# Performance work log

Measured on AMD Instinct MI355X. Metric: run time of the kernel, lower is better.

Reference implementation:

```python
import jax, jax.numpy as jnp
import numpy as np

EMBED_DIM = 1024
HEAD_NUM = 16
HEAD_DIM = 64


def setup_inputs() -> dict:
    key = jax.random.key(0)
    ks = jax.random.split(key, 9)
    B, S = 4, 4096
    sc = 1.0 / np.sqrt(HEAD_DIM)
    scf = 1.0 / np.sqrt(HEAD_NUM * HEAD_DIM)
    return {
        "value": jax.random.normal(ks[0], (B, S, EMBED_DIM), jnp.float32),
        "key": jax.random.normal(ks[1], (B, S, EMBED_DIM), jnp.float32),
        "query": jax.random.normal(ks[2], (B, S, EMBED_DIM), jnp.float32),
        "Wv": jax.random.normal(ks[3], (HEAD_DIM, HEAD_DIM), jnp.float32) * sc,
        "bv": jnp.zeros((HEAD_DIM,), jnp.float32),
        "Wk": jax.random.normal(ks[4], (HEAD_DIM, HEAD_DIM), jnp.float32) * sc,
        "bk": jnp.zeros((HEAD_DIM,), jnp.float32),
        "Wq": jax.random.normal(ks[5], (HEAD_DIM, HEAD_DIM), jnp.float32) * sc,
        "bq": jnp.zeros((HEAD_DIM,), jnp.float32),
        "Wfc": jax.random.normal(ks[6], (EMBED_DIM, HEAD_NUM * HEAD_DIM), jnp.float32) * scf,
        "bfc": jnp.zeros((EMBED_DIM,), jnp.float32),
    }


def reference(value, key, query, Wv, bv, Wk, bk, Wq, bq, Wfc, bfc):
    B, S, _ = value.shape
    H, D = HEAD_NUM, HEAD_DIM
    # reshape to [B, S, H, D]; per-head linear shares weights across heads
    v = value.reshape(B, S, H, D) @ Wv.T + bv
    k = key.reshape(B, S, H, D) @ Wk.T + bk
    q = query.reshape(B, S, H, D) @ Wq.T + bq
    # NOTE: faithful to original: attention over HEAD axis per position -> [B,S,H,H]
    energy = jnp.einsum("bshd,bsgd->bshg", q, k)
    attn = jax.nn.softmax(energy / jnp.sqrt(jnp.asarray(D, energy.dtype)), axis=-1)
    out = jnp.einsum("bshg,bsgd->bshd", attn, v).reshape(B, S, H * D)
    return out @ Wfc.T + bfc
```

## Files before the change

kernel.cpp:

```cpp
#include <hip/hip_runtime.h>
#include <hip/hip_bf16.h>

#define AS1 __attribute__((address_space(1)))
#define AS3 __attribute__((address_space(3)))

typedef __attribute__((ext_vector_type(8))) short bf16x8v;
typedef __attribute__((ext_vector_type(4))) short bf16x4v;
typedef __attribute__((ext_vector_type(4))) float f32x4;

__device__ __forceinline__ short f2bf(float f) {
  __hip_bfloat16 h = __float2bfloat16(f);
  return *reinterpret_cast<short*>(&h);
}
__device__ __forceinline__ bf16x4v cvt4(f32x4 v) {
  bf16x4v r; r[0]=f2bf(v[0]); r[1]=f2bf(v[1]); r[2]=f2bf(v[2]); r[3]=f2bf(v[3]);
  return r;
}
__device__ __forceinline__ bf16x8v cvt8(float4 a, float4 b) {
  bf16x8v r;
  r[0]=f2bf(a.x); r[1]=f2bf(a.y); r[2]=f2bf(a.z); r[3]=f2bf(a.w);
  r[4]=f2bf(b.x); r[5]=f2bf(b.y); r[6]=f2bf(b.z); r[7]=f2bf(b.w);
  return r;
}

__global__ void prep_kernel(const float* __restrict__ Wq, const float* __restrict__ Wk,
                            const float* __restrict__ Wv, const float* __restrict__ Wfc,
                            __hip_bfloat16* __restrict__ Wqb, __hip_bfloat16* __restrict__ Wkb,
                            __hip_bfloat16* __restrict__ Wvb, __hip_bfloat16* __restrict__ Wfcb)
{
  int i = blockIdx.x * blockDim.x + threadIdx.x;
  if (i < 64 * 64) {
    Wqb[i] = __float2bfloat16(Wq[i]);
    Wkb[i] = __float2bfloat16(Wk[i]);
    Wvb[i] = __float2bfloat16(Wv[i]);
  }
  for (int j = i; j < 1024 * 1024; j += gridDim.x * blockDim.x)
    Wfcb[j] = __float2bfloat16(Wfc[j]);
}

__global__ __launch_bounds__(256, 2) void attn_kernel(
    const float* __restrict__ Vin, const float* __restrict__ Kin,
    const float* __restrict__ Qin,
    const __hip_bfloat16* __restrict__ Wvb, const __hip_bfloat16* __restrict__ Wkb,
    const __hip_bfloat16* __restrict__ Wqb,
    const float* __restrict__ bv, const float* __restrict__ bk,
    const float* __restrict__ bq,
    __hip_bfloat16* __restrict__ Xout)
{
  const int wid = threadIdx.x >> 6, lane = threadIdx.x & 63;
  const int lo = lane & 15, hi = lane >> 4;
  const int tok0 = (blockIdx.x * 4 + wid) * 4;

  bf16x8v wqf[4][2], wkf[4][2], wvf[4][2];
#pragma unroll
  for (int i = 0; i < 4; ++i)
#pragma unroll
    for (int ks = 0; ks < 2; ++ks) {
      const int off = (i * 16 + lo) * 64 + ks * 32 + hi * 8;
      wqf[i][ks] = *(const bf16x8v*)(Wqb + off);
      wkf[i][ks] = *(const bf16x8v*)(Wkb + off);
      wvf[i][ks] = *(const bf16x8v*)(Wvb + off);
    }
  float4 bq4[4], bk4[4]; float bvv[4];
#pragma unroll
  for (int i = 0; i < 4; ++i) {
    bq4[i] = *(const float4*)(bq + i * 16 + hi * 4);
    bk4[i] = *(const float4*)(bk + i * 16 + hi * 4);
    bvv[i] = bv[i * 16 + lo];
  }

#pragma unroll 1
  for (int tl = 0; tl < 4; ++tl) {
    const size_t tb = (size_t)(tok0 + tl) * 1024;
    const float* qp = Qin + tb + lo * 64 + hi * 8;
    const float* kp = Kin + tb + lo * 64 + hi * 8;
    const float* vp = Vin + tb + lo * 64 + hi * 8;
    float4 qa0 = *(const float4*)(qp),      qb0 = *(const float4*)(qp + 4);
    float4 qa1 = *(const float4*)(qp + 32), qb1 = *(const float4*)(qp + 36);
    float4 ka0 = *(const float4*)(kp),      kb0 = *(const float4*)(kp + 4);
    float4 ka1 = *(const float4*)(kp + 32), kb1 = *(const float4*)(kp + 36);
    float4 va0 = *(const float4*)(vp),      vb0 = *(const float4*)(vp + 4);
    float4 va1 = *(const float4*)(vp + 32), vb1 = *(const float4*)(vp + 36);
    bf16x8v xq[2] = { cvt8(qa0, qb0), cvt8(qa1, qb1) };
    bf16x8v xk[2] = { cvt8(ka0, kb0), cvt8(ka1, kb1) };
    bf16x8v xv[2] = { cvt8(va0, vb0), cvt8(va1, vb1) };

    f32x4 qt[4], kt[4], vc[4];
#pragma unroll
    for (int i = 0; i < 4; ++i) {
      f32x4 aq = { bq4[i].x, bq4[i].y, bq4[i].z, bq4[i].w };
      aq = __builtin_amdgcn_mfma_f32_16x16x32_bf16(wqf[i][0], xq[0], aq, 0, 0, 0);
      aq = __builtin_amdgcn_mfma_f32_16x16x32_bf16(wqf[i][1], xq[1], aq, 0, 0, 0);
      qt[i] = aq;
      f32x4 ak = { bk4[i].x, bk4[i].y, bk4[i].z, bk4[i].w };
      ak = __builtin_amdgcn_mfma_f32_16x16x32_bf16(wkf[i][0], xk[0], ak, 0, 0, 0);
      ak = __builtin_amdgcn_mfma_f32_16x16x32_bf16(wkf[i][1], xk[1], ak, 0, 0, 0);
      kt[i] = ak;
    }
#pragma unroll
    for (int i = 0; i < 4; ++i) {
      f32x4 av = { bvv[i], bvv[i], bvv[i], bvv[i] };
      av = __builtin_amdgcn_mfma_f32_16x16x32_bf16(xv[0], wvf[i][0], av, 0, 0, 0);
      av = __builtin_amdgcn_mfma_f32_16x16x32_bf16(xv[1], wvf[i][1], av, 0, 0, 0);
      vc[i] = av;
    }

    f32x4 e = { 0.f, 0.f, 0.f, 0.f };
#pragma unroll
    for (int di = 0; di < 4; ++di)
      e = __builtin_amdgcn_mfma_f32_16x16x16bf16_1k(cvt4(kt[di]), cvt4(qt[di]), e, 0, 0, 0);

    float mx = fmaxf(fmaxf(e[0], e[1]), fmaxf(e[2], e[3]));
    mx = fmaxf(mx, __shfl_xor(mx, 16));
    mx = fmaxf(mx, __shfl_xor(mx, 32));
    float p0 = __expf((e[0] - mx) * 0.125f);
    float p1 = __expf((e[1] - mx) * 0.125f);
    float p2 = __expf((e[2] - mx) * 0.125f);
    float p3 = __expf((e[3] - mx) * 0.125f);
    float s = p0 + p1 + p2 + p3;
    s += __shfl_xor(s, 16);
    s += __shfl_xor(s, 32);
    const float inv = 1.0f / s;
    bf16x4v pa;
    pa[0] = f2bf(p0 * inv); pa[1] = f2bf(p1 * inv);
    pa[2] = f2bf(p2 * inv); pa[3] = f2bf(p3 * inv);

    __hip_bfloat16* xo = Xout + tb + (size_t)hi * 4 * 64 + lo;
#pragma unroll
    for (int ni = 0; ni < 4; ++ni) {
      f32x4 z = { 0.f, 0.f, 0.f, 0.f };
      z = __builtin_amdgcn_mfma_f32_16x16x16bf16_1k(pa, cvt4(vc[ni]), z, 0, 0, 0);
#pragma unroll
      for (int j = 0; j < 4; ++j)
        xo[j * 64 + ni * 16] = __float2bfloat16(z[j]);
    }
  }
}

__global__ __launch_bounds__(256) void gemm_kernel(
    const __hip_bfloat16* __restrict__ A,
    const __hip_bfloat16* __restrict__ B,
    const float* __restrict__ bias, float* __restrict__ C)
{
  constexpr int K = 1024, N = 1024;
  __shared__ __hip_bfloat16 Asm[128 * 64];
  __shared__ __hip_bfloat16 Bsm[128 * 64];
  const int tid = threadIdx.x, wid = tid >> 6, lane = tid & 63;
  const int bm = blockIdx.x >> 3, bn = blockIdx.x & 7;
  const int m0 = bm * 128, n0 = bn * 128;
  const int wr = wid >> 1, wc = wid & 1;

  f32x4 acc[4][4];
#pragma unroll
  for (int i = 0; i < 4; ++i)
#pragma unroll
    for (int j = 0; j < 4; ++j) acc[i][j] = (f32x4){0.f, 0.f, 0.f, 0.f};

  const int lrow = lane >> 3;
  const int gcol = ((lane & 7) ^ lrow) * 8;

  for (int kt = 0; kt < K / 64; ++kt) {
    const int k0 = kt * 64;
    __syncthreads();
#pragma unroll
    for (int c = 0; c < 4; ++c) {
      const int ca = wid * 4 + c;
      const int row = ca * 8 + lrow;
      __builtin_amdgcn_global_load_lds(
          (const AS1 void*)(A + (size_t)(m0 + row) * K + k0 + gcol),
          (AS3 void*)((char*)Asm + ca * 1024), 16, 0, 0);
      __builtin_amdgcn_global_load_lds(
          (const AS1 void*)(B + (size_t)(n0 + row) * K + k0 + gcol),
          (AS3 void*)((char*)Bsm + ca * 1024), 16, 0, 0);
    }
    asm volatile("s_waitcnt vmcnt(0)" ::: "memory");
    __syncthreads();

#pragma unroll
    for (int ks = 0; ks < 2; ++ks) {
      bf16x8v af[4], bfr[4];
#pragma unroll
      for (int mi = 0; mi < 4; ++mi) {
        const int arow = wr * 64 + mi * 16 + (lane & 15);
        const int slot = (ks * 4 + (lane >> 4)) ^ (arow & 7);
        af[mi] = *(const bf16x8v*)((const char*)Asm + arow * 128 + slot * 16);
      }
#pragma unroll
      for (int ni = 0; ni < 4; ++ni) {
        const int brow = wc * 64 + ni * 16 + (lane & 15);
        const int slot = (ks * 4 + (lane >> 4)) ^ (brow & 7);
        bfr[ni] = *(const bf16x8v*)((const char*)Bsm + brow * 128 + slot * 16);
      }
#pragma unroll
      for (int mi = 0; mi < 4; ++mi)
#pragma unroll
        for (int ni = 0; ni < 4; ++ni)
          acc[mi][ni] = __builtin_amdgcn_mfma_f32_16x16x32_bf16(
              af[mi], bfr[ni], acc[mi][ni], 0, 0, 0);
    }
  }

#pragma unroll
  for (int mi = 0; mi < 4; ++mi) {
    const int r0 = m0 + wr * 64 + mi * 16 + (lane >> 4) * 4;
#pragma unroll
    for (int ni = 0; ni < 4; ++ni) {
      const int c = n0 + wc * 64 + ni * 16 + (lane & 15);
      const float bs = bias[c];
#pragma unroll
      for (int j = 0; j < 4; ++j)
        C[(size_t)(r0 + j) * N + c] = acc[mi][ni][j] + bs;
    }
  }
}

extern "C" void kernel_launch(void* const* d_in, const int* in_sizes, int n_in,
                              void* d_out, int out_size, void* d_ws, size_t ws_size,
                              hipStream_t stream)
{
  const float* value = (const float*)d_in[0];
  const float* key   = (const float*)d_in[1];
  const float* query = (const float*)d_in[2];
  const float* Wv  = (const float*)d_in[3];
  const float* bv  = (const float*)d_in[4];
  const float* Wk  = (const float*)d_in[5];
  const float* bk  = (const float*)d_in[6];
  const float* Wq  = (const float*)d_in[7];
  const float* bq  = (const float*)d_in[8];
  const float* Wfc = (const float*)d_in[9];
  const float* bfc = (const float*)d_in[10];
  float* out = (float*)d_out;

  char* ws = (char*)d_ws;
  __hip_bfloat16* Xb   = (__hip_bfloat16*)ws;
  __hip_bfloat16* Wfcb = (__hip_bfloat16*)(ws + 33554432);
  __hip_bfloat16* Wqb  = (__hip_bfloat16*)(ws + 33554432 + 2097152);
  __hip_bfloat16* Wkb  = Wqb + 4096;
  __hip_bfloat16* Wvb  = Wkb + 4096;

  prep_kernel<<<4096, 256, 0, stream>>>(Wq, Wk, Wv, Wfc, Wqb, Wkb, Wvb, Wfcb);
  attn_kernel<<<1024, 256, 0, stream>>>(value, key, query, Wvb, Wkb, Wqb,
                                        bv, bk, bq, Xb);
  gemm_kernel<<<1024, 256, 0, stream>>>(Xb, Wfcb, bfc, out);
}
```

Measured before the change: 118.9 us.

## Stage per-head weights in LDS as pre-swizzled fragments to cut register pressure

The prep kernel now writes the Q/K/V weight matrices in an MFMA-fragment order. The attention kernel copies them into shared memory with global_load_lds and reads fragments from LDS each iteration, instead of holding 48 bf16x8 registers per lane. This frees VGPRs so more waves can run; the launch bound minimum of 2 blocks is dropped. It also splits the energy accumulation into two independent MFMA chains, moves the V projection after the softmax, and reorders the GEMM block index so consecutive blocks share the same N tile. The cost is extra LDS traffic per token and a barrier at kernel start.

```diff
diff --git a/kernel.cpp b/kernel.cpp
--- a/kernel.cpp
+++ b/kernel.cpp
@@ -7,6 +7,9 @@
 typedef __attribute__((ext_vector_type(8))) short bf16x8v;
 typedef __attribute__((ext_vector_type(4))) short bf16x4v;
 typedef __attribute__((ext_vector_type(4))) float f32x4;
+
+#define MFMA32 __builtin_amdgcn_mfma_f32_16x16x32_bf16
+#define MFMA16 __builtin_amdgcn_mfma_f32_16x16x16bf16_1k
 
 __device__ __forceinline__ short f2bf(float f) {
   __hip_bfloat16 h = __float2bfloat16(f);
@@ -25,42 +28,42 @@
 
 __global__ void prep_kernel(const float* __restrict__ Wq, const float* __restrict__ Wk,
                             const float* __restrict__ Wv, const float* __restrict__ Wfc,
-                            __hip_bfloat16* __restrict__ Wqb, __hip_bfloat16* __restrict__ Wkb,
-                            __hip_bfloat16* __restrict__ Wvb, __hip_bfloat16* __restrict__ Wfcb)
+                            __hip_bfloat16* __restrict__ Wfrag,
+                            __hip_bfloat16* __restrict__ Wfcb)
 {
   int i = blockIdx.x * blockDim.x + threadIdx.x;
   if (i < 64 * 64) {
-    Wqb[i] = __float2bfloat16(Wq[i]);
-    Wkb[i] = __float2bfloat16(Wk[i]);
-    Wvb[i] = __float2bfloat16(Wv[i]);
+    const int r = i >> 6, c = i & 63;
+    const int dst = (((r >> 4) * 2 + (c >> 5)) * 512) +
+                    ((((c >> 3) & 3) * 16 + (r & 15)) * 8) + (c & 7);
+    Wfrag[dst]        = __float2bfloat16(Wq[i]);
+    Wfrag[4096 + dst] = __float2bfloat16(Wk[i]);
+    Wfrag[8192 + dst] = __float2bfloat16(Wv[i]);
   }
   for (int j = i; j < 1024 * 1024; j += gridDim.x * blockDim.x)
     Wfcb[j] = __float2bfloat16(Wfc[j]);
 }
 
-__global__ __launch_bounds__(256, 2) void attn_kernel(
+__global__ __launch_bounds__(256) void attn_kernel(
     const float* __restrict__ Vin, const float* __restrict__ Kin,
     const float* __restrict__ Qin,
-    const __hip_bfloat16* __restrict__ Wvb, const __hip_bfloat16* __restrict__ Wkb,
-    const __hip_bfloat16* __restrict__ Wqb,
+    const __hip_bfloat16* __restrict__ Wfrag,
     const float* __restrict__ bv, const float* __restrict__ bk,
     const float* __restrict__ bq,
     __hip_bfloat16* __restrict__ Xout)
 {
+  __shared__ __hip_bfloat16 wlds[12288];
   const int wid = threadIdx.x >> 6, lane = threadIdx.x & 63;
   const int lo = lane & 15, hi = lane >> 4;
   const int tok0 = (blockIdx.x * 4 + wid) * 4;
-
-  bf16x8v wqf[4][2], wkf[4][2], wvf[4][2];
-#pragma unroll
-  for (int i = 0; i < 4; ++i)
-#pragma unroll
-    for (int ks = 0; ks < 2; ++ks) {
-      const int off = (i * 16 + lo) * 64 + ks * 32 + hi * 8;
-      wqf[i][ks] = *(const bf16x8v*)(Wqb + off);
-      wkf[i][ks] = *(const bf16x8v*)(Wkb + off);
-      wvf[i][ks] = *(const bf16x8v*)(Wvb + off);
-    }
+  const int xoff = lo * 64 + hi * 8;
+
+#pragma unroll
+  for (int c = 0; c < 6; ++c) {
+    const int ch = wid * 6 + c;
+    __builtin_amdgcn_global_load_lds((const AS1 void*)(Wfrag + ch * 512 + lane * 8),
+                                     (AS3 void*)(wlds + ch * 512), 16, 0, 0);
+  }
   float4 bq4[4], bk4[4]; float bvv[4];
 #pragma unroll
   for (int i = 0; i < 4; ++i) {
@@ -68,47 +71,53 @@
     bk4[i] = *(const float4*)(bk + i * 16 + hi * 4);
     bvv[i] = bv[i * 16 + lo];
   }
+  asm volatile("s_waitcnt vmcnt(0)" ::: "memory");
+  __syncthreads();
+
+  const char* wq_b = (const char*)wlds;
+  const char* wk_b = (const char*)(wlds + 4096);
+  const char* wv_b = (const char*)(wlds + 8192);
+  const int lb = lane * 16;
 
 #pragma unroll 1
-  for (int tl = 0; tl < 4; ++tl) {
-    const size_t tb = (size_t)(tok0 + tl) * 1024;
-    const float* qp = Qin + tb + lo * 64 + hi * 8;
-    const float* kp = Kin + tb + lo * 64 + hi * 8;
-    const float* vp = Vin + tb + lo * 64 + hi * 8;
+  for (int n = 0; n < 4; ++n) {
+    const size_t tb = (size_t)(tok0 + n) * 1024;
+    const float* qp = Qin + tb + xoff;
+    const float* kp = Kin + tb + xoff;
+    const float* vp = Vin + tb + xoff;
     float4 qa0 = *(const float4*)(qp),      qb0 = *(const float4*)(qp + 4);
     float4 qa1 = *(const float4*)(qp + 32), qb1 = *(const float4*)(qp + 36);
     float4 ka0 = *(const float4*)(kp),      kb0 = *(const float4*)(kp + 4);
     float4 ka1 = *(const float4*)(kp + 32), kb1 = *(const float4*)(kp + 36);
     float4 va0 = *(const float4*)(vp),      vb0 = *(const float4*)(vp + 4);
     float4 va1 = *(const float4*)(vp + 32), vb1 = *(const float4*)(vp + 36);
-    bf16x8v xq[2] = { cvt8(qa0, qb0), cvt8(qa1, qb1) };
-    bf16x8v xk[2] = { cvt8(ka0, kb0), cvt8(ka1, kb1) };
-    bf16x8v xv[2] = { cvt8(va0, vb0), cvt8(va1, vb1) };
-
-    f32x4 qt[4], kt[4], vc[4];
+    bf16x8v xq0 = cvt8(qa0, qb0), xq1 = cvt8(qa1, qb1);
+    bf16x8v xk0 = cvt8(ka0, kb0), xk1 = cvt8(ka1, kb1);
+    bf16x8v xv0 = cvt8(va0, vb0), xv1 = cvt8(va1, vb1);
+
+    f32x4 qt[4], kt[4];
 #pragma unroll
     for (int i = 0; i < 4; ++i) {
+      bf16x8v wq0 = *(const bf16x8v*)(wq_b + (i * 2 + 0) * 1024 + lb);
+      bf16x8v wq1 = *(const bf16x8v*)(wq_b + (i * 2 + 1) * 1024 + lb);
       f32x4 aq = { bq4[i].x, bq4[i].y, bq4[i].z, bq4[i].w };
-      aq = __builtin_amdgcn_mfma_f32_16x16x32_bf16(wqf[i][0], xq[0], aq, 0, 0, 0);
-      aq = __builtin_amdgcn_mfma_f32_16x16x32_bf16(wqf[i][1], xq[1], aq, 0, 0, 0);
+      aq = MFMA32(wq0, xq0, aq, 0, 0, 0);
+      aq = MFMA32(wq1, xq1, aq, 0, 0, 0);
       qt[i] = aq;
+      bf16x8v wk0 = *(const bf16x8v*)(wk_b + (i * 2 + 0) * 1024 + lb);
+      bf16x8v wk1 = *(const bf16x8v*)(wk_b + (i * 2 + 1) * 1024 + lb);
       f32x4 ak = { bk4[i].x, bk4[i].y, bk4[i].z, bk4[i].w };
-      ak = __builtin_amdgcn_mfma_f32_16x16x32_bf16(wkf[i][0], xk[0], ak, 0, 0, 0);
-      ak = __builtin_amdgcn_mfma_f32_16x16x32_bf16(wkf[i][1], xk[1], ak, 0, 0, 0);
+      ak = MFMA32(wk0, xk0, ak, 0, 0, 0);
+      ak = MFMA32(wk1, xk1, ak, 0, 0, 0);
       kt[i] = ak;
     }
-#pragma unroll
-    for (int i = 0; i < 4; ++i) {
-      f32x4 av = { bvv[i], bvv[i], bvv[i], bvv[i] };
-      av = __builtin_amdgcn_mfma_f32_16x16x32_bf16(xv[0], wvf[i][0], av, 0, 0, 0);
-      av = __builtin_amdgcn_mfma_f32_16x16x32_bf16(xv[1], wvf[i][1], av, 0, 0, 0);
-      vc[i] = av;
-    }
-
-    f32x4 e = { 0.f, 0.f, 0.f, 0.f };
-#pragma unroll
-    for (int di = 0; di < 4; ++di)
-      e = __builtin_amdgcn_mfma_f32_16x16x16bf16_1k(cvt4(kt[di]), cvt4(qt[di]), e, 0, 0, 0);
+
+    f32x4 ea = { 0.f, 0.f, 0.f, 0.f }, eb = { 0.f, 0.f, 0.f, 0.f };
+    ea = MFMA16(cvt4(kt[0]), cvt4(qt[0]), ea, 0, 0, 0);
+    eb = MFMA16(cvt4(kt[1]), cvt4(qt[1]), eb, 0, 0, 0);
+    ea = MFMA16(cvt4(kt[2]), cvt4(qt[2]), ea, 0, 0, 0);
+    eb = MFMA16(cvt4(kt[3]), cvt4(qt[3]), eb, 0, 0, 0);
+    f32x4 e = ea + eb;
 
     float mx = fmaxf(fmaxf(e[0], e[1]), fmaxf(e[2], e[3]));
     mx = fmaxf(mx, __shfl_xor(mx, 16));
@@ -125,11 +134,22 @@
     pa[0] = f2bf(p0 * inv); pa[1] = f2bf(p1 * inv);
     pa[2] = f2bf(p2 * inv); pa[3] = f2bf(p3 * inv);
 
+    f32x4 vc[4];
+#pragma unroll
+    for (int i = 0; i < 4; ++i) {
+      bf16x8v wv0 = *(const bf16x8v*)(wv_b + (i * 2 + 0) * 1024 + lb);
+      bf16x8v wv1 = *(const bf16x8v*)(wv_b + (i * 2 + 1) * 1024 + lb);
+      f32x4 av = { bvv[i], bvv[i], bvv[i], bvv[i] };
+      av = MFMA32(xv0, wv0, av, 0, 0, 0);
+      av = MFMA32(xv1, wv1, av, 0, 0, 0);
+      vc[i] = av;
+    }
+
     __hip_bfloat16* xo = Xout + tb + (size_t)hi * 4 * 64 + lo;
 #pragma unroll
     for (int ni = 0; ni < 4; ++ni) {
       f32x4 z = { 0.f, 0.f, 0.f, 0.f };
-      z = __builtin_amdgcn_mfma_f32_16x16x16bf16_1k(pa, cvt4(vc[ni]), z, 0, 0, 0);
+      z = MFMA16(pa, cvt4(vc[ni]), z, 0, 0, 0);
 #pragma unroll
       for (int j = 0; j < 4; ++j)
         xo[j * 64 + ni * 16] = __float2bfloat16(z[j]);
@@ -146,7 +166,7 @@
   __shared__ __hip_bfloat16 Asm[128 * 64];
   __shared__ __hip_bfloat16 Bsm[128 * 64];
   const int tid = threadIdx.x, wid = tid >> 6, lane = tid & 63;
-  const int bm = blockIdx.x >> 3, bn = blockIdx.x & 7;
+  const int bm = blockIdx.x & 127, bn = blockIdx.x >> 7;
   const int m0 = bm * 128, n0 = bn * 128;
   const int wr = wid >> 1, wc = wid & 1;
 
@@ -232,14 +252,12 @@
   float* out = (float*)d_out;
 
   char* ws = (char*)d_ws;
-  __hip_bfloat16* Xb   = (__hip_bfloat16*)ws;
-  __hip_bfloat16* Wfcb = (__hip_bfloat16*)(ws + 33554432);
-  __hip_bfloat16* Wqb  = (__hip_bfloat16*)(ws + 33554432 + 2097152);
-  __hip_bfloat16* Wkb  = Wqb + 4096;
-  __hip_bfloat16* Wvb  = Wkb + 4096;
-
-  prep_kernel<<<4096, 256, 0, stream>>>(Wq, Wk, Wv, Wfc, Wqb, Wkb, Wvb, Wfcb);
-  attn_kernel<<<1024, 256, 0, stream>>>(value, key, query, Wvb, Wkb, Wqb,
+  __hip_bfloat16* Xb    = (__hip_bfloat16*)ws;
+  __hip_bfloat16* Wfcb  = (__hip_bfloat16*)(ws + 33554432);
+  __hip_bfloat16* Wfrag = (__hip_bfloat16*)(ws + 33554432 + 2097152);
+
+  prep_kernel<<<4096, 256, 0, stream>>>(Wq, Wk, Wv, Wfc, Wfrag, Wfcb);
+  attn_kernel<<<1024, 256, 0, stream>>>(value, key, query, Wfrag,
                                         bv, bk, bq, Xb);
   gemm_kernel<<<1024, 256, 0, stream>>>(Xb, Wfcb, bfc, out);
 }
```

Result: faster. 104.4 us (-12.2%).
